# Kernel optimization log

Measured on AMD Instinct MI355X. Metric: run time of the kernel, lower is better.

Reference implementation:

```python
import jax, jax.numpy as jnp
import numpy as np

B, C, H, W = 32, 256, 32, 32
K, HEADS, U, V = 16, 4, 1, 64  # dim_depth, heads, dim_u, dim_v = dim_out//heads
R = 23
PAD = (R - 1) // 2
EPS = 1e-5


def setup_inputs() -> dict:
    key = jax.random.key(0)
    ks = jax.random.split(key, 10)
    return {
        "x": jax.random.normal(ks[0], (B, C, H, W), jnp.float32),
        "Wq": jax.random.normal(ks[1], (K * HEADS, C), jnp.float32) * (1.0 / np.sqrt(C)),
        "bn_q_w": jax.random.uniform(ks[2], (K * HEADS,), jnp.float32, 0.5, 1.5),
        "bn_q_b": jax.random.normal(ks[3], (K * HEADS,), jnp.float32) * 0.1,
        "Wk": jax.random.normal(ks[4], (K * U, C), jnp.float32) * (1.0 / np.sqrt(C)),
        "Wv": jax.random.normal(ks[5], (V * U, C), jnp.float32) * (1.0 / np.sqrt(C)),
        "bn_v_w": jax.random.uniform(ks[6], (V * U,), jnp.float32, 0.5, 1.5),
        "bn_v_b": jax.random.normal(ks[7], (V * U,), jnp.float32) * 0.1,
        "embedding": jax.random.normal(ks[8], (K, U, 1, R, R), jnp.float32),
        "gamma": jax.random.normal(ks[9], (1,), jnp.float32),
    }


def _conv1x1(x, w):
    # x: [b,c,h,w], w: [o,c] -> [b,o,h,w]
    return jnp.einsum('bchw,oc->bohw', x, w)


def _bn(x, w, b):
    # training-mode BatchNorm2d: batch stats over (b,h,w) per channel
    mean = jnp.mean(x, axis=(0, 2, 3), keepdims=True)
    var = jnp.var(x, axis=(0, 2, 3), keepdims=True)
    xn = (x - mean) * jax.lax.rsqrt(var + EPS)
    return xn * w[None, :, None, None] + b[None, :, None, None]


def reference(x, Wq, bn_q_w, bn_q_b, Wk, Wv, bn_v_w, bn_v_b, embedding, gamma):
    b, c, h, w = x.shape
    n = h * w
    queries = _bn(_conv1x1(x, Wq), bn_q_w, bn_q_b).reshape(b, HEADS, K, n)        # bhkn
    softmax = jax.nn.softmax(_conv1x1(x, Wk).reshape(b, K, U, n), axis=-1)         # bkun
    values = _bn(_conv1x1(x, Wv), bn_v_w, bn_v_b).reshape(b, V, U, n)              # bvun

    # content lambda
    lambda_c = jnp.einsum('bkun,bvun->bkv', softmax, values)
    y_c = jnp.einsum('bhkn,bkv->bhvn', queries, lambda_c)

    # position lambda via conv3d over (V, H, W) with kernel (1, R, R)
    v5 = jnp.transpose(values, (0, 2, 1, 3)).reshape(b, U, V, h, w)                # NCDHW, C=U, D=V
    lambda_p = jax.lax.conv_general_dilated(
        v5, embedding,
        window_strides=(1, 1, 1),
        padding=((0, 0), (PAD, PAD), (PAD, PAD)),
        dimension_numbers=('NCDHW', 'OIDHW', 'NCDHW'))                              # [b,K,V,h,w]
    lambda_p = lambda_p.reshape(b, K, V, n)
    y_p = jnp.einsum('bhkn,bkvn->bhvn', queries, lambda_p)

    out = (y_c + y_p).reshape(b, HEADS * V, h, w)
    out = out + gamma * out
    return out
```

## Files before the change

### kernel.cpp

```cpp
#include <hip/hip_runtime.h>
#include <math.h>

#define BB 32
#define CC 256
#define NPIX 1024
#define KD 16
#define NHEADS 4
#define VDIM 64
#define RR 23
#define PADR 11
#define EPSBN 1e-5f

typedef short short8v __attribute__((ext_vector_type(8)));
typedef short short4v __attribute__((ext_vector_type(4)));
typedef float floatx4 __attribute__((ext_vector_type(4)));

__device__ __forceinline__ unsigned short f2bf(float f) {
  union { float f; unsigned u; } c; c.f = f;
  unsigned u = c.u;
  return (unsigned short)((u + 0x7FFFu + ((u >> 16) & 1u)) >> 16);
}
__device__ __forceinline__ float bf2f(unsigned short h) {
  union { unsigned u; float f; } c; c.u = ((unsigned)h) << 16;
  return c.f;
}

#define NINV (1.0f / 32768.0f)

__global__ __launch_bounds__(256) void k_prep(const float* __restrict__ emb,
    unsigned short* __restrict__ embA,
    const float* __restrict__ Wq, const float* __restrict__ Wk,
    const float* __restrict__ Wv, unsigned short* __restrict__ wA,
    float* __restrict__ raw, float* __restrict__ lcG) {
  int bid = blockIdx.x;
  if (bid == 0) raw[threadIdx.x] = 0.f;
  if (bid < 46) {
    int l = bid * 256 + threadIdx.x;
    if (l >= 23 * 16 * 32) return;
    int dr = l >> 9, rem = l & 511;
    int m = rem >> 5, kd = rem & 31;
    unsigned short val = 0;
    if (kd < 23) val = f2bf(emb[(size_t)m * 529 + dr * 23 + kd]);
    embA[l] = val;
  } else if (bid < 190) {
    int idx = (bid - 46) * 256 + threadIdx.x;
    int j = idx & 7, lane = (idx >> 3) & 63, ks = (idx >> 9) & 7, ot = idx >> 12;
    int o = ot * 16 + (lane & 15);
    int c = ks * 32 + (lane >> 4) * 8 + j;
    const float* src = (o < 64) ? (Wq + (size_t)o * CC)
                     : (o < 80) ? (Wk + (size_t)(o - 64) * CC)
                                : (Wv + (size_t)(o - 80) * CC);
    wA[idx] = f2bf(src[c]);
  } else {
    lcG[(bid - 190) * 256 + threadIdx.x] = 0.f;
  }
}

__global__ __launch_bounds__(256) void k_proj(const float* __restrict__ x,
    const unsigned short* __restrict__ wA,
    float* __restrict__ q_pre, float* __restrict__ k_pre, float* __restrict__ v_pre,
    float* __restrict__ raw) {
  __shared__ float ssum[144], ssq[144];
  int b = blockIdx.y;
  int t = threadIdx.x;
  int s = t >> 6;
  int lane = t & 63;
  int nl = lane & 15, quad = lane >> 4;
  int pix = blockIdx.x * 64 + s * 16 + nl;

  if (t < 144) { ssum[t] = 0.f; ssq[t] = 0.f; }
  __syncthreads();

  const float* xb = x + ((size_t)b * CC) * NPIX + pix;
  const unsigned short* ap = wA + lane * 8;

  floatx4 acc[9];
#pragma unroll
  for (int i = 0; i < 9; ++i) acc[i] = (floatx4){0.f, 0.f, 0.f, 0.f};

#pragma unroll
  for (int ks = 0; ks < 8; ++ks) {
    union { short8v v; unsigned short u[8]; } bb;
    const float* xc = xb + ((size_t)(ks * 32 + quad * 8)) * NPIX;
#pragma unroll
    for (int j = 0; j < 8; ++j) bb.u[j] = f2bf(xc[(size_t)j * NPIX]);
#pragma unroll
    for (int ot = 0; ot < 9; ++ot) {
      short8v af = *(const short8v*)(ap + ((ot * 8 + ks) << 9));
      acc[ot] = __builtin_amdgcn_mfma_f32_16x16x32_bf16(af, bb.v, acc[ot], 0, 0, 0);
    }
  }

#pragma unroll
  for (int ot = 0; ot < 9; ++ot) {
#pragma unroll
    for (int r = 0; r < 4; ++r) {
      int o = ot * 16 + quad * 4 + r;
      float val = acc[ot][r];
      if (o < 64)      q_pre[((size_t)b * 64 + o) * NPIX + pix] = val;
      else if (o < 80) k_pre[((size_t)b * 16 + (o - 64)) * NPIX + pix] = val;
      else             v_pre[((size_t)b * 64 + (o - 80)) * NPIX + pix] = val;
    }
  }

#pragma unroll
  for (int ot = 0; ot < 9; ++ot) {
#pragma unroll
    for (int r = 0; r < 4; ++r) {
      int o = ot * 16 + quad * 4 + r;
      if (o >= 64 && o < 80) continue;
      float v1 = acc[ot][r];
      float v2 = v1 * v1;
#pragma unroll
      for (int m = 1; m < 16; m <<= 1) {
        v1 += __shfl_xor(v1, m);
        v2 += __shfl_xor(v2, m);
      }
      if (nl == 0) {
        atomicAdd(&ssum[o], v1);
        atomicAdd(&ssq[o], v2);
      }
    }
  }
  __syncthreads();
  if (t < 64) {
    atomicAdd(&raw[t], ssum[t]);
    atomicAdd(&raw[64 + t], ssq[t]);
  } else if (t < 128) {
    atomicAdd(&raw[64 + t], ssum[t + 16]);
    atomicAdd(&raw[192 + (t - 64)], ssq[t + 16]);
  }
}

__global__ __launch_bounds__(256) void k_nvsm(float* __restrict__ vn,
    const float* __restrict__ raw,
    const float* __restrict__ bn_v_w, const float* __restrict__ bn_v_b,
    const float* __restrict__ k_pre, float* __restrict__ p) {
  __shared__ float vsc[64], vsh[64];
  __shared__ float shm[4], shs[4];
  int b = blockIdx.y, bx = blockIdx.x, t = threadIdx.x;
  if (bx < 16) {
    if (t < 64) {
      float mean = raw[128 + t] * NINV;
      float var = raw[192 + t] * NINV - mean * mean;
      float sc = rsqrtf(var + EPSBN) * bn_v_w[t];
      vsc[t] = sc;
      vsh[t] = bn_v_b[t] - mean * sc;
    }
    __syncthreads();
    int n0 = bx * 64;
    for (int l = t; l < 4096; l += 256) {
      int o = l >> 6, nn = l & 63;
      size_t a = ((size_t)b * 64 + o) * NPIX + n0 + nn;
      vn[a] = fmaf(vn[a], vsc[o], vsh[o]);
    }
  } else {
    int k = bx - 16;
    const float* src = k_pre + ((size_t)b * 16 + k) * NPIX;
    float v[4];
    float mx = -1e30f;
#pragma unroll
    for (int i = 0; i < 4; ++i) { v[i] = src[t + 256 * i]; mx = fmaxf(mx, v[i]); }
#pragma unroll
    for (int off = 32; off > 0; off >>= 1) mx = fmaxf(mx, __shfl_down(mx, off));
    if ((t & 63) == 0) shm[t >> 6] = mx;
    __syncthreads();
    mx = fmaxf(fmaxf(shm[0], shm[1]), fmaxf(shm[2], shm[3]));
    float s = 0.f;
#pragma unroll
    for (int i = 0; i < 4; ++i) { v[i] = __expf(v[i] - mx); s += v[i]; }
#pragma unroll
    for (int off = 32; off > 0; off >>= 1) s += __shfl_down(s, off);
    if ((t & 63) == 0) shs[t >> 6] = s;
    __syncthreads();
    float r = 1.0f / (shs[0] + shs[1] + shs[2] + shs[3]);
    float* dst = p + ((size_t)b * 16 + k) * NPIX;
#pragma unroll
    for (int i = 0; i < 4; ++i) dst[t + 256 * i] = v[i] * r;
  }
}

#define IMG_RS 68
#define IMG_CS 3728
#define LAM_RS 1032

union KMainLDS {
  short imgc[4 * IMG_CS];
  short lam[16 * LAM_RS];
};

__device__ __forceinline__ short8v ld_win(const short* p) {
  union { short8v s8; short4v s4[2]; } bu;
  bu.s4[0] = *(const short4v*)p;
  bu.s4[1] = *(const short4v*)(p + 4);
  return bu.s8;
}

__global__ __launch_bounds__(256, 3) void k_conv(const float* __restrict__ vn,
    const float* __restrict__ p, const unsigned short* __restrict__ embA,
    unsigned short* __restrict__ lamG, float* __restrict__ lcG) {
  __shared__ __align__(16) KMainLDS u;
  int b = blockIdx.y, bx = blockIdx.x, t = threadIdx.x;
  int lane = t & 63, wv = t >> 6;

  if (bx >= 64) {
    int nc = bx - 64, n0 = nc * 64;
    float* pl = (float*)u.imgc;
    float* vl = pl + 16 * 64;
    for (int l = t; l < 1024; l += 256) {
      int k = l >> 6, nn = l & 63;
      pl[k * 64 + nn] = p[((size_t)b * 16 + k) * NPIX + n0 + nn];
    }
    for (int l = t; l < 4096; l += 256) {
      int v64 = l >> 6, nn = l & 63;
      vl[v64 * 65 + nn] = vn[((size_t)b * 64 + v64) * NPIX + n0 + nn];
    }
    __syncthreads();
    int k = t >> 4, v4 = (t & 15) * 4;
    float a0 = 0.f, a1 = 0.f, a2 = 0.f, a3 = 0.f;
    const float* pk = &pl[k * 64];
#pragma unroll 8
    for (int i = 0; i < 64; ++i) {
      float pv = pk[i];
      a0 = fmaf(pv, vl[(v4 + 0) * 65 + i], a0);
      a1 = fmaf(pv, vl[(v4 + 1) * 65 + i], a1);
      a2 = fmaf(pv, vl[(v4 + 2) * 65 + i], a2);
      a3 = fmaf(pv, vl[(v4 + 3) * 65 + i], a3);
    }
    float* dst = lcG + (size_t)b * 1024 + k * 64 + v4;
    atomicAdd(dst + 0, a0); atomicAdd(dst + 1, a1);
    atomicAdd(dst + 2, a2); atomicAdd(dst + 3, a3);
    return;
  }

  int v = bx;
  int4* z4 = (int4*)u.imgc;
  for (int l = t; l < 1864; l += 256) z4[l] = make_int4(0, 0, 0, 0);
  __syncthreads();

  const float* vsrc = vn + ((size_t)b * 64 + v) * NPIX;
  for (int l = t; l < 512; l += 256) {
    int pix = l * 2;
    int y = pix >> 5, xx = pix & 31;
    float2 vv = *(const float2*)(vsrc + pix);
    unsigned short h0 = f2bf(vv.x), h1 = f2bf(vv.y);
#pragma unroll
    for (int s = 0; s < 4; ++s) {
      int base = s * IMG_CS + (y + PADR) * IMG_RS + xx + PADR + s;
      u.imgc[base] = (short)h0;
      u.imgc[base + 1] = (short)h1;
    }
  }
  __syncthreads();

  int nl = lane & 15, quad = lane >> 4;
  int y0 = wv * 8;
  int scopy = (4 - (nl & 3)) & 3;
  int colbase = scopy * IMG_CS + nl + quad * 8 + scopy;
  const unsigned short* aptr = embA + nl * 32 + quad * 8;

  floatx4 acc[16];
#pragma unroll
  for (int i = 0; i < 16; ++i) acc[i] = (floatx4){0.f, 0.f, 0.f, 0.f};

  short8v bfrag[8][2];
#pragma unroll
  for (int rr = 0; rr < 8; ++rr) {
    const short* rp = &u.imgc[(y0 + rr) * IMG_RS + colbase];
    bfrag[rr][0] = ld_win(rp);
    bfrag[rr][1] = ld_win(rp + 16);
  }

  short8v a0 = *(const short8v*)aptr;
  short8v a1 = *(const short8v*)(aptr + 512);
#pragma unroll
  for (int dr = 0; dr < RR; ++dr) {
    short8v afrag = a0;
    a0 = a1;
    if (dr < RR - 2) a1 = *(const short8v*)(aptr + (dr + 2) * 512);
#pragma unroll
    for (int rr = 0; rr < 8; ++rr) {
      int slot = (dr + rr) & 7;
      acc[rr * 2 + 0] = __builtin_amdgcn_mfma_f32_16x16x32_bf16(afrag, bfrag[slot][0], acc[rr * 2 + 0], 0, 0, 0);
      acc[rr * 2 + 1] = __builtin_amdgcn_mfma_f32_16x16x32_bf16(afrag, bfrag[slot][1], acc[rr * 2 + 1], 0, 0, 0);
    }
    if (dr < RR - 1) {
      const short* rp = &u.imgc[(y0 + dr + 8) * IMG_RS + colbase];
      int slot = dr & 7;
      bfrag[slot][0] = ld_win(rp);
      bfrag[slot][1] = ld_win(rp + 16);
    }
  }

  __syncthreads();
#pragma unroll
  for (int tt = 0; tt < 16; ++tt) {
    int y = y0 + (tt >> 1), c0 = (tt & 1) << 4;
    int pix = y * 32 + c0 + nl;
#pragma unroll
    for (int r = 0; r < 4; ++r)
      u.lam[(quad * 4 + r) * LAM_RS + pix] = (short)f2bf(acc[tt][r]);
  }
  __syncthreads();

  uint4* dst = (uint4*)(lamG + ((size_t)(b * 64 + v)) * 16 * 1024);
  for (int idx = t; idx < 2048; idx += 256) {
    int row = idx >> 7, col = idx & 127;
    dst[row * 128 + col] = *(const uint4*)&u.lam[row * LAM_RS + col * 8];
  }
}

__global__ __launch_bounds__(256) void k_epi2(const unsigned short* __restrict__ lamG,
    const float* __restrict__ q_pre, const float* __restrict__ raw,
    const float* __restrict__ bn_q_w, const float* __restrict__ bn_q_b,
    const float* __restrict__ lcG,
    const float* __restrict__ gamma, float* __restrict__ out) {
  __shared__ float qs[64 * 64];
  __shared__ float lcs[1024];
  __shared__ float qsc[64], qsh[64];
  int b = blockIdx.y, nc = blockIdx.x, z = blockIdx.z, t = threadIdx.x;
  if (t < 64) {
    float mean = raw[t] * NINV;
    float var = raw[64 + t] * NINV - mean * mean;
    float sc = rsqrtf(var + EPSBN) * bn_q_w[t];
    qsc[t] = sc;
    qsh[t] = bn_q_b[t] - mean * sc;
  }
  for (int l = t; l < 1024; l += 256) lcs[l] = lcG[(size_t)b * 1024 + l];
  __syncthreads();
  int n0 = nc * 64;
  for (int l = t; l < 4096; l += 256) {
    int o = l >> 6, nn = l & 63;
    qs[l] = fmaf(q_pre[((size_t)b * 64 + o) * NPIX + n0 + nn], qsc[o], qsh[o]);
  }
  __syncthreads();
  float g1 = 1.0f + gamma[0];
  int p0 = (t & 15) * 4;
  int g = t >> 4;
#pragma unroll
  for (int vi = 0; vi < 2; ++vi) {
    int v = z * 32 + vi * 16 + g;
    const unsigned short* ls = lamG + ((size_t)(b * 64 + v)) * 16 * 1024 + n0 + p0;
    float yacc[4][4];
#pragma unroll
    for (int h = 0; h < 4; ++h)
#pragma unroll
      for (int i = 0; i < 4; ++i) yacc[h][i] = 0.f;
#pragma unroll
    for (int k = 0; k < 16; ++k) {
      uint2 w = *(const uint2*)(ls + k * 1024);
      float lv = lcs[k * 64 + v];
      float l0 = bf2f((unsigned short)(w.x & 0xffffu)) + lv;
      float l1 = bf2f((unsigned short)(w.x >> 16)) + lv;
      float l2 = bf2f((unsigned short)(w.y & 0xffffu)) + lv;
      float l3 = bf2f((unsigned short)(w.y >> 16)) + lv;
#pragma unroll
      for (int h = 0; h < 4; ++h) {
        const float* qrow = &qs[(h * 16 + k) * 64 + p0];
        yacc[h][0] = fmaf(qrow[0], l0, yacc[h][0]);
        yacc[h][1] = fmaf(qrow[1], l1, yacc[h][1]);
        yacc[h][2] = fmaf(qrow[2], l2, yacc[h][2]);
        yacc[h][3] = fmaf(qrow[3], l3, yacc[h][3]);
      }
    }
#pragma unroll
    for (int h = 0; h < 4; ++h) {
      float4 r;
      r.x = g1 * yacc[h][0]; r.y = g1 * yacc[h][1];
      r.z = g1 * yacc[h][2]; r.w = g1 * yacc[h][3];
      *(float4*)&out[((size_t)b * 256 + h * 64 + v) * NPIX + n0 + p0] = r;
    }
  }
}

__global__ __launch_bounds__(256, 3) void k_fused(const float* __restrict__ vn,
    const float* __restrict__ q_pre, const float* __restrict__ raw,
    const float* __restrict__ bn_q_w, const float* __restrict__ bn_q_b,
    const float* __restrict__ p, const unsigned short* __restrict__ embA,
    const float* __restrict__ gamma, float* __restrict__ out) {
  __shared__ __align__(16) KMainLDS u;
  __shared__ float lcv[16];
  __shared__ float red[256];
  __shared__ float qsc[64], qsh[64];
  int b = blockIdx.y, v = blockIdx.x, t = threadIdx.x;

  int4* z4 = (int4*)u.imgc;
  for (int l = t; l < 1864; l += 256) z4[l] = make_int4(0, 0, 0, 0);
  if (t < 64) {
    float mean = raw[t] * NINV;
    float var = raw[64 + t] * NINV - mean * mean;
    float sc = rsqrtf(var + EPSBN) * bn_q_w[t];
    qsc[t] = sc;
    qsh[t] = bn_q_b[t] - mean * sc;
  }
  {
    int kk = t & 15, ch = t >> 4;
    const float* pp = p + ((size_t)b * 16 + kk) * NPIX + ch * 64;
    const float* vv = vn + ((size_t)b * 64 + v) * NPIX + ch * 64;
    float part = 0.f;
#pragma unroll 8
    for (int i = 0; i < 64; ++i) part = fmaf(pp[i], vv[i], part);
    red[t] = part;
  }
  __syncthreads();
  if (t < 16) {
    float s = 0.f;
#pragma unroll
    for (int c = 0; c < 16; ++c) s += red[c * 16 + t];
    lcv[t] = s;
  }

  const float* vsrc = vn + ((size_t)b * 64 + v) * NPIX;
  for (int l = t; l < 512; l += 256) {
    int pix = l * 2;
    int y = pix >> 5, xx = pix & 31;
    float2 vv = *(const float2*)(vsrc + pix);
    unsigned short h0 = f2bf(vv.x), h1 = f2bf(vv.y);
#pragma unroll
    for (int s = 0; s < 4; ++s) {
      int base = s * IMG_CS + (y + PADR) * IMG_RS + xx + PADR + s;
      u.imgc[base] = (short)h0;
      u.imgc[base + 1] = (short)h1;
    }
  }
  __syncthreads();

  int lane = t & 63, wv = t >> 6;
  int nl = lane & 15, quad = lane >> 4;
  int y0 = wv * 8;
  int scopy = (4 - (nl & 3)) & 3;
  int colbase = scopy * IMG_CS + nl + quad * 8 + scopy;
  const unsigned short* aptr = embA + nl * 32 + quad * 8;

  floatx4 acc[16];
#pragma unroll
  for (int i = 0; i < 16; ++i) acc[i] = (floatx4){0.f, 0.f, 0.f, 0.f};

  short8v bfrag[8][2];
#pragma unroll
  for (int rr = 0; rr < 8; ++rr) {
    const short* rp = &u.imgc[(y0 + rr) * IMG_RS + colbase];
    bfrag[rr][0] = ld_win(rp);
    bfrag[rr][1] = ld_win(rp + 16);
  }

  short8v a0 = *(const short8v*)aptr;
  short8v a1 = *(const short8v*)(aptr + 512);
#pragma unroll
  for (int dr = 0; dr < RR; ++dr) {
    short8v afrag = a0;
    a0 = a1;
    if (dr < RR - 2) a1 = *(const short8v*)(aptr + (dr + 2) * 512);
#pragma unroll
    for (int rr = 0; rr < 8; ++rr) {
      int slot = (dr + rr) & 7;
      acc[rr * 2 + 0] = __builtin_amdgcn_mfma_f32_16x16x32_bf16(afrag, bfrag[slot][0], acc[rr * 2 + 0], 0, 0, 0);
      acc[rr * 2 + 1] = __builtin_amdgcn_mfma_f32_16x16x32_bf16(afrag, bfrag[slot][1], acc[rr * 2 + 1], 0, 0, 0);
    }
    if (dr < RR - 1) {
      const short* rp = &u.imgc[(y0 + dr + 8) * IMG_RS + colbase];
      int slot = dr & 7;
      bfrag[slot][0] = ld_win(rp);
      bfrag[slot][1] = ld_win(rp + 16);
    }
  }

  __syncthreads();
#pragma unroll
  for (int tt = 0; tt < 16; ++tt) {
    int y = y0 + (tt >> 1), c0 = (tt & 1) << 4;
    int pix = y * 32 + c0 + nl;
#pragma unroll
    for (int r = 0; r < 4; ++r)
      u.lam[(quad * 4 + r) * LAM_RS + pix] = (short)f2bf(acc[tt][r] + lcv[quad * 4 + r]);
  }
  __syncthreads();

  int p0 = t * 4;
  float yacc[4][4];
#pragma unroll
  for (int h = 0; h < 4; ++h)
#pragma unroll
    for (int i = 0; i < 4; ++i) yacc[h][i] = 0.f;
  const float* qb = q_pre + ((size_t)b * 64) * NPIX + p0;
#pragma unroll
  for (int k = 0; k < 16; ++k) {
    uint2 w = *(const uint2*)&u.lam[k * LAM_RS + p0];
    float l0 = bf2f((unsigned short)(w.x & 0xffffu));
    float l1 = bf2f((unsigned short)(w.x >> 16));
    float l2 = bf2f((unsigned short)(w.y & 0xffffu));
    float l3 = bf2f((unsigned short)(w.y >> 16));
#pragma unroll
    for (int h = 0; h < 4; ++h) {
      int o = h * 16 + k;
      float4 qv = *(const float4*)(qb + (size_t)o * NPIX);
      yacc[h][0] = fmaf(fmaf(qv.x, qsc[o], qsh[o]), l0, yacc[h][0]);
      yacc[h][1] = fmaf(fmaf(qv.y, qsc[o], qsh[o]), l1, yacc[h][1]);
      yacc[h][2] = fmaf(fmaf(qv.z, qsc[o], qsh[o]), l2, yacc[h][2]);
      yacc[h][3] = fmaf(fmaf(qv.w, qsc[o], qsh[o]), l3, yacc[h][3]);
    }
  }
  float g1 = 1.0f + gamma[0];
#pragma unroll
  for (int h = 0; h < 4; ++h) {
    float4 r;
    r.x = g1 * yacc[h][0]; r.y = g1 * yacc[h][1];
    r.z = g1 * yacc[h][2]; r.w = g1 * yacc[h][3];
    *(float4*)&out[((size_t)b * 256 + h * 64 + v) * NPIX + p0] = r;
  }
}

extern "C" void kernel_launch(void* const* d_in, const int* in_sizes, int n_in,
                              void* d_out, int out_size, void* d_ws, size_t ws_size,
                              hipStream_t stream) {
  const float* x      = (const float*)d_in[0];
  const float* Wq     = (const float*)d_in[1];
  const float* bn_q_w = (const float*)d_in[2];
  const float* bn_q_b = (const float*)d_in[3];
  const float* Wk     = (const float*)d_in[4];
  const float* Wv     = (const float*)d_in[5];
  const float* bn_v_w = (const float*)d_in[6];
  const float* bn_v_b = (const float*)d_in[7];
  const float* emb    = (const float*)d_in[8];
  const float* gamma  = (const float*)d_in[9];
  float* out = (float*)d_out;

  float* ws    = (float*)d_ws;
  float* q_pre = ws;
  float* k_pre = q_pre + (size_t)BB * 64 * NPIX;
  float* vn    = k_pre + (size_t)BB * 16 * NPIX;
  float* p     = vn    + (size_t)BB * 64 * NPIX;
  float* raw   = p     + (size_t)BB * 16 * NPIX;
  float* lcG   = raw + 256;
  unsigned short* embA = (unsigned short*)(lcG + (size_t)BB * 1024);
  unsigned short* wA   = embA + 23 * 16 * 32;
  unsigned short* lamG = wA + 144 * 256;

  size_t need = ((size_t)(lamG - (unsigned short*)ws)) * 2
              + (size_t)BB * 64 * 16 * NPIX * 2;

  k_prep  <<<dim3(318),       256, 0, stream>>>(emb, embA, Wq, Wk, Wv, wA, raw, lcG);
  k_proj  <<<dim3(16, BB),    256, 0, stream>>>(x, wA, q_pre, k_pre, vn, raw);
  k_nvsm  <<<dim3(32, BB),    256, 0, stream>>>(vn, raw, bn_v_w, bn_v_b, k_pre, p);
  if (ws_size >= need) {
    k_conv<<<dim3(80, BB),    256, 0, stream>>>(vn, p, embA, lamG, lcG);
    k_epi2<<<dim3(16, BB, 2), 256, 0, stream>>>(lamG, q_pre, raw, bn_q_w, bn_q_b, lcG, gamma, out);
  } else {
    k_fused<<<dim3(64, BB),   256, 0, stream>>>(vn, q_pre, raw, bn_q_w, bn_q_b, p, embA, gamma, out);
  }
}
```

Baseline: 210.9 us.

## Fold V batch-norm and softmax into conv kernel, dropping the normalize pass

Removes the k_nvsm launch on the main path. Value batch-norm is now applied on the fly when k_conv loads vn. The softmax is computed as an unnormalized exp with per-row sums accumulated atomically into a new esum buffer, and the 1/sum factor is applied to lambda_c in k_epi2. This avoids a full read/write pass over vn and p. It skips the max-subtraction in the softmax, which risks overflow for large logits. k_epi2 is also split across 4 z-slices instead of 2 for more parallelism.

```diff
diff --git a/kernel.cpp b/kernel.cpp
--- a/kernel.cpp
+++ b/kernel.cpp
@@ -31,7 +31,7 @@
     unsigned short* __restrict__ embA,
     const float* __restrict__ Wq, const float* __restrict__ Wk,
     const float* __restrict__ Wv, unsigned short* __restrict__ wA,
-    float* __restrict__ raw, float* __restrict__ lcG) {
+    float* __restrict__ raw, float* __restrict__ lcG, float* __restrict__ esum) {
   int bid = blockIdx.x;
   if (bid == 0) raw[threadIdx.x] = 0.f;
   if (bid < 46) {
@@ -51,8 +51,10 @@
                      : (o < 80) ? (Wk + (size_t)(o - 64) * CC)
                                 : (Wv + (size_t)(o - 80) * CC);
     wA[idx] = f2bf(src[c]);
+  } else if (bid < 318) {
+    lcG[(bid - 190) * 256 + threadIdx.x] = 0.f;
   } else {
-    lcG[(bid - 190) * 256 + threadIdx.x] = 0.f;
+    esum[(bid - 318) * 256 + threadIdx.x] = 0.f;
   }
 }
 
@@ -129,6 +131,223 @@
   } else if (t < 128) {
     atomicAdd(&raw[64 + t], ssum[t + 16]);
     atomicAdd(&raw[192 + (t - 64)], ssq[t + 16]);
+  }
+}
+
+#define IMG_RS 68
+#define IMG_CS 3728
+#define LAM_RS 1032
+
+union KMainLDS {
+  short imgc[4 * IMG_CS];
+  short lam[16 * LAM_RS];
+};
+
+__device__ __forceinline__ short8v ld_win(const short* p) {
+  union { short8v s8; short4v s4[2]; } bu;
+  bu.s4[0] = *(const short4v*)p;
+  bu.s4[1] = *(const short4v*)(p + 4);
+  return bu.s8;
+}
+
+__global__ __launch_bounds__(256, 3) void k_conv(const float* __restrict__ vn,
+    const float* __restrict__ k_pre, const float* __restrict__ raw,
+    const float* __restrict__ bn_v_w, const float* __restrict__ bn_v_b,
+    const unsigned short* __restrict__ embA,
+    unsigned short* __restrict__ lamG, float* __restrict__ lcG,
+    float* __restrict__ esum) {
+  __shared__ __align__(16) KMainLDS u;
+  int b = blockIdx.y, bx = blockIdx.x, t = threadIdx.x;
+  int lane = t & 63, wv = t >> 6;
+
+  if (bx >= 64) {
+    int nc = bx - 64, n0 = nc * 64;
+    float* pl = (float*)u.imgc;
+    float* vl = pl + 16 * 64;
+    float* vscb = vl + 64 * 65;
+    float* vshb = vscb + 64;
+    if (t < 64) {
+      float mean = raw[128 + t] * NINV;
+      float var = raw[192 + t] * NINV - mean * mean;
+      float sc = rsqrtf(var + EPSBN) * bn_v_w[t];
+      vscb[t] = sc;
+      vshb[t] = bn_v_b[t] - mean * sc;
+    }
+    for (int l = t; l < 1024; l += 256) {
+      int k = l >> 6, nn = l & 63;
+      pl[l] = __expf(k_pre[((size_t)b * 16 + k) * NPIX + n0 + nn]);
+    }
+    __syncthreads();
+    {
+      int k = t >> 4, j = t & 15;
+      const float* pk = &pl[k * 64 + j * 4];
+      float s = pk[0] + pk[1] + pk[2] + pk[3];
+#pragma unroll
+      for (int m = 1; m < 16; m <<= 1) s += __shfl_xor(s, m);
+      if (j == 0) atomicAdd(&esum[b * 16 + k], s);
+    }
+    for (int l = t; l < 4096; l += 256) {
+      int v64 = l >> 6, nn = l & 63;
+      vl[v64 * 65 + nn] = fmaf(vn[((size_t)b * 64 + v64) * NPIX + n0 + nn],
+                               vscb[v64], vshb[v64]);
+    }
+    __syncthreads();
+    int k = t >> 4, v4 = (t & 15) * 4;
+    float a0 = 0.f, a1 = 0.f, a2 = 0.f, a3 = 0.f;
+    const float* pk = &pl[k * 64];
+#pragma unroll 8
+    for (int i = 0; i < 64; ++i) {
+      float pv = pk[i];
+      a0 = fmaf(pv, vl[(v4 + 0) * 65 + i], a0);
+      a1 = fmaf(pv, vl[(v4 + 1) * 65 + i], a1);
+      a2 = fmaf(pv, vl[(v4 + 2) * 65 + i], a2);
+      a3 = fmaf(pv, vl[(v4 + 3) * 65 + i], a3);
+    }
+    float* dst = lcG + (size_t)b * 1024 + k * 64 + v4;
+    atomicAdd(dst + 0, a0); atomicAdd(dst + 1, a1);
+    atomicAdd(dst + 2, a2); atomicAdd(dst + 3, a3);
+    return;
+  }
+
+  int v = bx;
+  int4* z4 = (int4*)u.imgc;
+  for (int l = t; l < 1864; l += 256) z4[l] = make_int4(0, 0, 0, 0);
+  float vmean = raw[128 + v] * NINV;
+  float vvar = raw[192 + v] * NINV - vmean * vmean;
+  float vsc = rsqrtf(vvar + EPSBN) * bn_v_w[v];
+  float vsh = bn_v_b[v] - vmean * vsc;
+  __syncthreads();
+
+  const float* vsrc = vn + ((size_t)b * 64 + v) * NPIX;
+  for (int l = t; l < 512; l += 256) {
+    int pix = l * 2;
+    int y = pix >> 5, xx = pix & 31;
+    float2 vv = *(const float2*)(vsrc + pix);
+    unsigned short h0 = f2bf(fmaf(vv.x, vsc, vsh));
+    unsigned short h1 = f2bf(fmaf(vv.y, vsc, vsh));
+#pragma unroll
+    for (int s = 0; s < 4; ++s) {
+      int base = s * IMG_CS + (y + PADR) * IMG_RS + xx + PADR + s;
+      u.imgc[base] = (short)h0;
+      u.imgc[base + 1] = (short)h1;
+    }
+  }
+  __syncthreads();
+
+  int nl = lane & 15, quad = lane >> 4;
+  int y0 = wv * 8;
+  int scopy = (4 - (nl & 3)) & 3;
+  int colbase = scopy * IMG_CS + nl + quad * 8 + scopy;
+  const unsigned short* aptr = embA + nl * 32 + quad * 8;
+
+  floatx4 acc[16];
+#pragma unroll
+  for (int i = 0; i < 16; ++i) acc[i] = (floatx4){0.f, 0.f, 0.f, 0.f};
+
+  short8v bfrag[8][2];
+#pragma unroll
+  for (int rr = 0; rr < 8; ++rr) {
+    const short* rp = &u.imgc[(y0 + rr) * IMG_RS + colbase];
+    bfrag[rr][0] = ld_win(rp);
+    bfrag[rr][1] = ld_win(rp + 16);
+  }
+
+  short8v a0 = *(const short8v*)aptr;
+  short8v a1 = *(const short8v*)(aptr + 512);
+#pragma unroll
+  for (int dr = 0; dr < RR; ++dr) {
+    short8v afrag = a0;
+    a0 = a1;
+    if (dr < RR - 2) a1 = *(const short8v*)(aptr + (dr + 2) * 512);
+#pragma unroll
+    for (int rr = 0; rr < 8; ++rr) {
+      int slot = (dr + rr) & 7;
+      acc[rr * 2 + 0] = __builtin_amdgcn_mfma_f32_16x16x32_bf16(afrag, bfrag[slot][0], acc[rr * 2 + 0], 0, 0, 0);
+      acc[rr * 2 + 1] = __builtin_amdgcn_mfma_f32_16x16x32_bf16(afrag, bfrag[slot][1], acc[rr * 2 + 1], 0, 0, 0);
+    }
+    if (dr < RR - 1) {
+      const short* rp = &u.imgc[(y0 + dr + 8) * IMG_RS + colbase];
+      int slot = dr & 7;
+      bfrag[slot][0] = ld_win(rp);
+      bfrag[slot][1] = ld_win(rp + 16);
+    }
+  }
+
+  __syncthreads();
+#pragma unroll
+  for (int tt = 0; tt < 16; ++tt) {
+    int y = y0 + (tt >> 1), c0 = (tt & 1) << 4;
+    int pix = y * 32 + c0 + nl;
+#pragma unroll
+    for (int r = 0; r < 4; ++r)
+      u.lam[(quad * 4 + r) * LAM_RS + pix] = (short)f2bf(acc[tt][r]);
+  }
+  __syncthreads();
+
+  uint4* dst = (uint4*)(lamG + ((size_t)(b * 64 + v)) * 16 * 1024);
+  for (int idx = t; idx < 2048; idx += 256) {
+    int row = idx >> 7, col = idx & 127;
+    dst[row * 128 + col] = *(const uint4*)&u.lam[row * LAM_RS + col * 8];
+  }
+}
+
+__global__ __launch_bounds__(256) void k_epi2(const unsigned short* __restrict__ lamG,
+    const float* __restrict__ q_pre, const float* __restrict__ raw,
+    const float* __restrict__ bn_q_w, const float* __restrict__ bn_q_b,
+    const float* __restrict__ lcG, const float* __restrict__ esum,
+    const float* __restrict__ gamma, float* __restrict__ out) {
+  __shared__ float qs[64 * 64];
+  __shared__ float lcs[1024];
+  __shared__ float qsc[64], qsh[64], rkv[16];
+  int b = blockIdx.y, nc = blockIdx.x, z = blockIdx.z, t = threadIdx.x;
+  if (t < 64) {
+    float mean = raw[t] * NINV;
+    float var = raw[64 + t] * NINV - mean * mean;
+    float sc = rsqrtf(var + EPSBN) * bn_q_w[t];
+    qsc[t] = sc;
+    qsh[t] = bn_q_b[t] - mean * sc;
+  }
+  if (t < 16) rkv[t] = 1.0f / esum[b * 16 + t];
+  __syncthreads();
+  for (int l = t; l < 1024; l += 256) lcs[l] = lcG[(size_t)b * 1024 + l] * rkv[l >> 6];
+  int n0 = nc * 64;
+  for (int l = t; l < 4096; l += 256) {
+    int o = l >> 6, nn = l & 63;
+    qs[l] = fmaf(q_pre[((size_t)b * 64 + o) * NPIX + n0 + nn], qsc[o], qsh[o]);
+  }
+  __syncthreads();
+  float g1 = 1.0f + gamma[0];
+  int p0 = (t & 15) * 4;
+  int v = z * 16 + (t >> 4);
+  const unsigned short* ls = lamG + ((size_t)(b * 64 + v)) * 16 * 1024 + n0 + p0;
+  float yacc[4][4];
+#pragma unroll
+  for (int h = 0; h < 4; ++h)
+#pragma unroll
+    for (int i = 0; i < 4; ++i) yacc[h][i] = 0.f;
+#pragma unroll
+  for (int k = 0; k < 16; ++k) {
+    uint2 w = *(const uint2*)(ls + k * 1024);
+    float lv = lcs[k * 64 + v];
+    float l0 = bf2f((unsigned short)(w.x & 0xffffu)) + lv;
+    float l1 = bf2f((unsigned short)(w.x >> 16)) + lv;
+    float l2 = bf2f((unsigned short)(w.y & 0xffffu)) + lv;
+    float l3 = bf2f((unsigned short)(w.y >> 16)) + lv;
+#pragma unroll
+    for (int h = 0; h < 4; ++h) {
+      const float* qrow = &qs[(h * 16 + k) * 64 + p0];
+      yacc[h][0] = fmaf(qrow[0], l0, yacc[h][0]);
+      yacc[h][1] = fmaf(qrow[1], l1, yacc[h][1]);
+      yacc[h][2] = fmaf(qrow[2], l2, yacc[h][2]);
+      yacc[h][3] = fmaf(qrow[3], l3, yacc[h][3]);
+    }
+  }
+#pragma unroll
+  for (int h = 0; h < 4; ++h) {
+    float4 r;
+    r.x = g1 * yacc[h][0]; r.y = g1 * yacc[h][1];
+    r.z = g1 * yacc[h][2]; r.w = g1 * yacc[h][3];
+    *(float4*)&out[((size_t)b * 256 + h * 64 + v) * NPIX + n0 + p0] = r;
   }
 }
 
@@ -180,199 +399,6 @@
   }
 }
 
-#define IMG_RS 68
-#define IMG_CS 3728
-#define LAM_RS 1032
-
-union KMainLDS {
-  short imgc[4 * IMG_CS];
-  short lam[16 * LAM_RS];
-};
-
-__device__ __forceinline__ short8v ld_win(const short* p) {
-  union { short8v s8; short4v s4[2]; } bu;
-  bu.s4[0] = *(const short4v*)p;
-  bu.s4[1] = *(const short4v*)(p + 4);
-  return bu.s8;
-}
-
-__global__ __launch_bounds__(256, 3) void k_conv(const float* __restrict__ vn,
-    const float* __restrict__ p, const unsigned short* __restrict__ embA,
-    unsigned short* __restrict__ lamG, float* __restrict__ lcG) {
-  __shared__ __align__(16) KMainLDS u;
-  int b = blockIdx.y, bx = blockIdx.x, t = threadIdx.x;
-  int lane = t & 63, wv = t >> 6;
-
-  if (bx >= 64) {
-    int nc = bx - 64, n0 = nc * 64;
-    float* pl = (float*)u.imgc;
-    float* vl = pl + 16 * 64;
-    for (int l = t; l < 1024; l += 256) {
-      int k = l >> 6, nn = l & 63;
-      pl[k * 64 + nn] = p[((size_t)b * 16 + k) * NPIX + n0 + nn];
-    }
-    for (int l = t; l < 4096; l += 256) {
-      int v64 = l >> 6, nn = l & 63;
-      vl[v64 * 65 + nn] = vn[((size_t)b * 64 + v64) * NPIX + n0 + nn];
-    }
-    __syncthreads();
-    int k = t >> 4, v4 = (t & 15) * 4;
-    float a0 = 0.f, a1 = 0.f, a2 = 0.f, a3 = 0.f;
-    const float* pk = &pl[k * 64];
-#pragma unroll 8
-    for (int i = 0; i < 64; ++i) {
-      float pv = pk[i];
-      a0 = fmaf(pv, vl[(v4 + 0) * 65 + i], a0);
-      a1 = fmaf(pv, vl[(v4 + 1) * 65 + i], a1);
-      a2 = fmaf(pv, vl[(v4 + 2) * 65 + i], a2);
-      a3 = fmaf(pv, vl[(v4 + 3) * 65 + i], a3);
-    }
-    float* dst = lcG + (size_t)b * 1024 + k * 64 + v4;
-    atomicAdd(dst + 0, a0); atomicAdd(dst + 1, a1);
-    atomicAdd(dst + 2, a2); atomicAdd(dst + 3, a3);
-    return;
-  }
-
-  int v = bx;
-  int4* z4 = (int4*)u.imgc;
-  for (int l = t; l < 1864; l += 256) z4[l] = make_int4(0, 0, 0, 0);
-  __syncthreads();
-
-  const float* vsrc = vn + ((size_t)b * 64 + v) * NPIX;
-  for (int l = t; l < 512; l += 256) {
-    int pix = l * 2;
-    int y = pix >> 5, xx = pix & 31;
-    float2 vv = *(const float2*)(vsrc + pix);
-    unsigned short h0 = f2bf(vv.x), h1 = f2bf(vv.y);
-#pragma unroll
-    for (int s = 0; s < 4; ++s) {
-      int base = s * IMG_CS + (y + PADR) * IMG_RS + xx + PADR + s;
-      u.imgc[base] = (short)h0;
-      u.imgc[base + 1] = (short)h1;
-    }
-  }
-  __syncthreads();
-
-  int nl = lane & 15, quad = lane >> 4;
-  int y0 = wv * 8;
-  int scopy = (4 - (nl & 3)) & 3;
-  int colbase = scopy * IMG_CS + nl + quad * 8 + scopy;
-  const unsigned short* aptr = embA + nl * 32 + quad * 8;
-
-  floatx4 acc[16];
-#pragma unroll
-  for (int i = 0; i < 16; ++i) acc[i] = (floatx4){0.f, 0.f, 0.f, 0.f};
-
-  short8v bfrag[8][2];
-#pragma unroll
-  for (int rr = 0; rr < 8; ++rr) {
-    const short* rp = &u.imgc[(y0 + rr) * IMG_RS + colbase];
-    bfrag[rr][0] = ld_win(rp);
-    bfrag[rr][1] = ld_win(rp + 16);
-  }
-
-  short8v a0 = *(const short8v*)aptr;
-  short8v a1 = *(const short8v*)(aptr + 512);
-#pragma unroll
-  for (int dr = 0; dr < RR; ++dr) {
-    short8v afrag = a0;
-    a0 = a1;
-    if (dr < RR - 2) a1 = *(const short8v*)(aptr + (dr + 2) * 512);
-#pragma unroll
-    for (int rr = 0; rr < 8; ++rr) {
-      int slot = (dr + rr) & 7;
-      acc[rr * 2 + 0] = __builtin_amdgcn_mfma_f32_16x16x32_bf16(afrag, bfrag[slot][0], acc[rr * 2 + 0], 0, 0, 0);
-      acc[rr * 2 + 1] = __builtin_amdgcn_mfma_f32_16x16x32_bf16(afrag, bfrag[slot][1], acc[rr * 2 + 1], 0, 0, 0);
-    }
-    if (dr < RR - 1) {
-      const short* rp = &u.imgc[(y0 + dr + 8) * IMG_RS + colbase];
-      int slot = dr & 7;
-      bfrag[slot][0] = ld_win(rp);
-      bfrag[slot][1] = ld_win(rp + 16);
-    }
-  }
-
-  __syncthreads();
-#pragma unroll
-  for (int tt = 0; tt < 16; ++tt) {
-    int y = y0 + (tt >> 1), c0 = (tt & 1) << 4;
-    int pix = y * 32 + c0 + nl;
-#pragma unroll
-    for (int r = 0; r < 4; ++r)
-      u.lam[(quad * 4 + r) * LAM_RS + pix] = (short)f2bf(acc[tt][r]);
-  }
-  __syncthreads();
-
-  uint4* dst = (uint4*)(lamG + ((size_t)(b * 64 + v)) * 16 * 1024);
-  for (int idx = t; idx < 2048; idx += 256) {
-    int row = idx >> 7, col = idx & 127;
-    dst[row * 128 + col] = *(const uint4*)&u.lam[row * LAM_RS + col * 8];
-  }
-}
-
-__global__ __launch_bounds__(256) void k_epi2(const unsigned short* __restrict__ lamG,
-    const float* __restrict__ q_pre, const float* __restrict__ raw,
-    const float* __restrict__ bn_q_w, const float* __restrict__ bn_q_b,
-    const float* __restrict__ lcG,
-    const float* __restrict__ gamma, float* __restrict__ out) {
-  __shared__ float qs[64 * 64];
-  __shared__ float lcs[1024];
-  __shared__ float qsc[64], qsh[64];
-  int b = blockIdx.y, nc = blockIdx.x, z = blockIdx.z, t = threadIdx.x;
-  if (t < 64) {
-    float mean = raw[t] * NINV;
-    float var = raw[64 + t] * NINV - mean * mean;
-    float sc = rsqrtf(var + EPSBN) * bn_q_w[t];
-    qsc[t] = sc;
-    qsh[t] = bn_q_b[t] - mean * sc;
-  }
-  for (int l = t; l < 1024; l += 256) lcs[l] = lcG[(size_t)b * 1024 + l];
-  __syncthreads();
-  int n0 = nc * 64;
-  for (int l = t; l < 4096; l += 256) {
-    int o = l >> 6, nn = l & 63;
-    qs[l] = fmaf(q_pre[((size_t)b * 64 + o) * NPIX + n0 + nn], qsc[o], qsh[o]);
-  }
-  __syncthreads();
-  float g1 = 1.0f + gamma[0];
-  int p0 = (t & 15) * 4;
-  int g = t >> 4;
-#pragma unroll
-  for (int vi = 0; vi < 2; ++vi) {
-    int v = z * 32 + vi * 16 + g;
-    const unsigned short* ls = lamG + ((size_t)(b * 64 + v)) * 16 * 1024 + n0 + p0;
-    float yacc[4][4];
-#pragma unroll
-    for (int h = 0; h < 4; ++h)
-#pragma unroll
-      for (int i = 0; i < 4; ++i) yacc[h][i] = 0.f;
-#pragma unroll
-    for (int k = 0; k < 16; ++k) {
-      uint2 w = *(const uint2*)(ls + k * 1024);
-      float lv = lcs[k * 64 + v];
-      float l0 = bf2f((unsigned short)(w.x & 0xffffu)) + lv;
-      float l1 = bf2f((unsigned short)(w.x >> 16)) + lv;
-      float l2 = bf2f((unsigned short)(w.y & 0xffffu)) + lv;
-      float l3 = bf2f((unsigned short)(w.y >> 16)) + lv;
-#pragma unroll
-      for (int h = 0; h < 4; ++h) {
-        const float* qrow = &qs[(h * 16 + k) * 64 + p0];
-        yacc[h][0] = fmaf(qrow[0], l0, yacc[h][0]);
-        yacc[h][1] = fmaf(qrow[1], l1, yacc[h][1]);
-        yacc[h][2] = fmaf(qrow[2], l2, yacc[h][2]);
-        yacc[h][3] = fmaf(qrow[3], l3, yacc[h][3]);
-      }
-    }
-#pragma unroll
-    for (int h = 0; h < 4; ++h) {
-      float4 r;
-      r.x = g1 * yacc[h][0]; r.y = g1 * yacc[h][1];
-      r.z = g1 * yacc[h][2]; r.w = g1 * yacc[h][3];
-      *(float4*)&out[((size_t)b * 256 + h * 64 + v) * NPIX + n0 + p0] = r;
-    }
-  }
-}
-
 __global__ __launch_bounds__(256, 3) void k_fused(const float* __restrict__ vn,
     const float* __restrict__ q_pre, const float* __restrict__ raw,
     const float* __restrict__ bn_q_w, const float* __restrict__ bn_q_b,
@@ -532,20 +558,21 @@
   float* p     = vn    + (size_t)BB * 64 * NPIX;
   float* raw   = p     + (size_t)BB * 16 * NPIX;
   float* lcG   = raw + 256;
-  unsigned short* embA = (unsigned short*)(lcG + (size_t)BB * 1024);
+  float* esum  = lcG + (size_t)BB * 1024;
+  unsigned short* embA = (unsigned short*)(esum + BB * 32);
   unsigned short* wA   = embA + 23 * 16 * 32;
   unsigned short* lamG = wA + 144 * 256;
 
   size_t need = ((size_t)(lamG - (unsigned short*)ws)) * 2
               + (size_t)BB * 64 * 16 * NPIX * 2;
 
-  k_prep  <<<dim3(318),       256, 0, stream>>>(emb, embA, Wq, Wk, Wv, wA, raw, lcG);
+  k_prep  <<<dim3(320),       256, 0, stream>>>(emb, embA, Wq, Wk, Wv, wA, raw, lcG, esum);
   k_proj  <<<dim3(16, BB),    256, 0, stream>>>(x, wA, q_pre, k_pre, vn, raw);
-  k_nvsm  <<<dim3(32, BB),    256, 0, stream>>>(vn, raw, bn_v_w, bn_v_b, k_pre, p);
   if (ws_size >= need) {
-    k_conv<<<dim3(80, BB),    256, 0, stream>>>(vn, p, embA, lamG, lcG);
-    k_epi2<<<dim3(16, BB, 2), 256, 0, stream>>>(lamG, q_pre, raw, bn_q_w, bn_q_b, lcG, gamma, out);
+    k_conv<<<dim3(80, BB),    256, 0, stream>>>(vn, k_pre, raw, bn_v_w, bn_v_b, embA, lamG, lcG, esum);
+    k_epi2<<<dim3(16, BB, 4), 256, 0, stream>>>(lamG, q_pre, raw, bn_q_w, bn_q_b, lcG, esum, gamma, out);
   } else {
+    k_nvsm<<<dim3(32, BB),    256, 0, stream>>>(vn, raw, bn_v_w, bn_v_b, k_pre, p);
     k_fused<<<dim3(64, BB),   256, 0, stream>>>(vn, q_pre, raw, bn_q_w, bn_q_b, p, embA, gamma, out);
   }
 }
```

Result: faster. 185.6 us (median of 2 runs) (-12.0%).
